# Kernel optimization log

Hardware: AMD Instinct MI355X
Metric: run time of the kernel (lower is better)

## Reference

```python
import jax, jax.numpy as jnp
import numpy as np

NUM_HEADS = 16
GROUP_SIZE = 4
RMS_EPS = 1e-6


def _rope_cos_sin(S, head_dim):
    # matches compute_freqs_cis: freqs = 1/10000**(arange(0,hd,2)/hd), angles = outer(t, freqs)
    inv_freq = 1.0 / (10000.0 ** (jnp.arange(0, head_dim, 2, dtype=jnp.float32) / head_dim))
    t = jnp.arange(S, dtype=jnp.float32)
    angles = t[:, None] * inv_freq[None, :]          # [S, hd/2]
    return jnp.cos(angles), jnp.sin(angles)


def _apply_rope(x, cos, sin):
    # x: [B, S, h, hd]; complex multiply on (even, odd) pairs
    B, S, h, hd = x.shape
    xr = x.reshape(B, S, h, hd // 2, 2)
    x0, x1 = xr[..., 0], xr[..., 1]
    c = cos[None, :, None, :]
    s = sin[None, :, None, :]
    o0 = x0 * c - x1 * s
    o1 = x0 * s + x1 * c
    return jnp.stack([o0, o1], axis=-1).reshape(B, S, h, hd)


def setup_inputs() -> dict:
    key = jax.random.key(0)
    k1, k2, k3 = jax.random.split(key, 3)
    B, S, H = 4, 2048, 2048
    g = GROUP_SIZE
    x = jax.random.normal(k1, (B, S, H), dtype=jnp.float32)
    w_attn = jax.random.normal(k2, (H, H + 2 * H // g), dtype=jnp.float32) * 0.02
    w_proj = jax.random.normal(k3, (H, H), dtype=jnp.float32) * 0.02
    norm_w = jnp.ones((H,), dtype=jnp.float32)
    return {"x": x, "w_attn": w_attn, "w_proj": w_proj, "norm_w": norm_w}


def reference(x, w_attn, w_proj, norm_w):
    B, S, H = x.shape
    nh = NUM_HEADS
    g = GROUP_SIZE
    nkv = nh // g
    hd = H // nh
    ghd = H // g

    qkv = jnp.einsum('bsh,hf->bsf', x, w_attn)
    q = qkv[..., :H].reshape(B, S, nh, hd)
    k = qkv[..., H:H + ghd].reshape(B, S, nkv, hd)
    v = qkv[..., H + ghd:].reshape(B, S, nkv, hd)

    cos, sin = _rope_cos_sin(S, hd)
    q = _apply_rope(q, cos, sin)
    k = _apply_rope(k, cos, sin)

    q = q.transpose(0, 2, 1, 3)                      # [B, nh, S, hd]
    k = jnp.repeat(k.transpose(0, 2, 1, 3), g, axis=1)   # [B, nh, S, hd]
    v = jnp.repeat(v.transpose(0, 2, 1, 3), g, axis=1)

    scale = 1.0 / jnp.sqrt(jnp.float32(hd))
    scores = jnp.einsum('bhqd,bhkd->bhqk', q, k) * scale
    causal = jnp.tril(jnp.ones((S, S), dtype=bool))
    scores = jnp.where(causal[None, None], scores, jnp.finfo(scores.dtype).min)
    attn = jax.nn.softmax(scores, axis=-1)
    y = jnp.einsum('bhqk,bhkd->bhqd', attn, v)       # [B, nh, S, hd]
    y = y.transpose(0, 2, 1, 3).reshape(B, S, H)

    y = jnp.einsum('bsh,ho->bso', y, w_proj)
    # RMSNorm
    rms = jnp.sqrt(jnp.mean(jnp.square(y), axis=-1, keepdims=True) + RMS_EPS)
    return (y / rms) * norm_w
```

## Files before the change

kernel.cpp:

```cpp
#include <hip/hip_runtime.h>

#define DEVI __device__ __forceinline__

using u16 = unsigned short;
using u32 = unsigned int;

typedef __attribute__((ext_vector_type(8))) short short8v;
typedef __attribute__((ext_vector_type(4))) float f32x4;
typedef __attribute__((ext_vector_type(2))) u32 u32x2;

DEVI u16 f2b(float f) {
  u32 u = __builtin_bit_cast(u32, f);
  u += 0x7fffu + ((u >> 16) & 1u);
  return (u16)(u >> 16);
}
DEVI float b2f(u16 b) { return __builtin_bit_cast(float, (u32)b << 16); }

DEVI void gload16(const void* g, void* l) {
  __builtin_amdgcn_global_load_lds(
      (const __attribute__((address_space(1))) void*)g,
      (__attribute__((address_space(3))) void*)l, 16, 0, 0);
}

__global__ __launch_bounds__(256) void cvt_x_k(const float* __restrict__ in,
                                               u16* __restrict__ out) {
  size_t i = ((size_t)blockIdx.x * 256 + threadIdx.x) * 8;
  f32x4 a = *(const f32x4*)(in + i);
  f32x4 c = *(const f32x4*)(in + i + 4);
  short8v o;
  o[0] = (short)f2b(a[0]); o[1] = (short)f2b(a[1]);
  o[2] = (short)f2b(a[2]); o[3] = (short)f2b(a[3]);
  o[4] = (short)f2b(c[0]); o[5] = (short)f2b(c[1]);
  o[6] = (short)f2b(c[2]); o[7] = (short)f2b(c[3]);
  *(short8v*)(out + i) = o;
}

__global__ __launch_bounds__(256) void transpose_cvt_k(
    const float* __restrict__ in, u16* __restrict__ out, int R, int Ccols) {
  __shared__ u16 tile[64][65];
  const int r0 = blockIdx.y * 64, c0 = blockIdx.x * 64;
  const int tx = threadIdx.x & 63, ty = threadIdx.x >> 6;
#pragma unroll
  for (int jj = 0; jj < 16; ++jj) {
    int r = ty + jj * 4;
    tile[r][tx] = f2b(in[(size_t)(r0 + r) * Ccols + c0 + tx]);
  }
  __syncthreads();
#pragma unroll
  for (int jj = 0; jj < 16; ++jj) {
    int c = ty + jj * 4;
    out[(size_t)(c0 + c) * R + r0 + tx] = tile[tx][c];
  }
}

__global__ __launch_bounds__(256) void rope_table_k(float* __restrict__ cosT,
                                                    float* __restrict__ sinT) {
  int idx = blockIdx.x * 256 + threadIdx.x;
  int s = idx >> 6, i = idx & 63;
  float inv_freq = expf(-(float)i * (1.0f / 64.0f) * 9.210340371976184f);
  float ang = (float)s * inv_freq;
  cosT[idx] = cosf(ang);
  sinT[idx] = sinf(ang);
}

__global__ __launch_bounds__(256) void rope_scatter_k(
    const u16* __restrict__ qkv, const float* __restrict__ cosT,
    const float* __restrict__ sinT, u16* __restrict__ q_r,
    u16* __restrict__ k_r) {
  const float QS = 0.08838834764831845f * 1.4426950408889634f;
  const int row = blockIdx.x;
  const int b = row >> 11, s = row & 2047;
  const u16* in = qkv + (size_t)row * 3072;
  const float* cp = cosT + s * 64;
  const float* sp = sinT + s * 64;
  for (int p = threadIdx.x; p < 1280; p += 256) {
    int f0 = p * 2;
    u32 pair = *(const u32*)(in + f0);
    float x0 = b2f((u16)(pair & 0xffffu));
    float x1 = b2f((u16)(pair >> 16));
    int d, head;
    u16* dst;
    bool isq = (f0 < 2048);
    if (isq) {
      head = f0 >> 7; d = f0 & 127;
      dst = q_r + (((size_t)(b * 16 + head)) * 2048 + s) * 128 + d;
    } else {
      int idx = f0 - 2048;
      head = idx >> 7; d = idx & 127;
      dst = k_r + (((size_t)(b * 4 + head)) * 2048 + s) * 128 + d;
    }
    int i = d >> 1;
    float c = cp[i], sn = sp[i];
    float o0 = x0 * c - x1 * sn;
    float o1 = x0 * sn + x1 * c;
    if (isq) { o0 *= QS; o1 *= QS; }
    *(u32*)dst = (u32)f2b(o0) | ((u32)f2b(o1) << 16);
  }
}

__global__ __launch_bounds__(256) void v_trans_k(const u16* __restrict__ qkv,
                                                 u16* __restrict__ vT) {
  __shared__ u16 tile[64][65];
  const int s0 = blockIdx.x * 64, d0 = blockIdx.y * 64;
  const int bk = blockIdx.z;
  const int b = bk >> 2, kh = bk & 3;
  const int tx = threadIdx.x & 63, ty = threadIdx.x >> 6;
  const u16* src = qkv + ((size_t)b * 2048) * 3072 + 2560 + kh * 128;
#pragma unroll
  for (int jj = 0; jj < 16; ++jj) {
    int s = ty + jj * 4;
    tile[s][tx] = src[(size_t)(s0 + s) * 3072 + d0 + tx];
  }
  __syncthreads();
  u16* dst = vT + (((size_t)bk * 128 + d0) * 2048) + s0;
#pragma unroll
  for (int jj = 0; jj < 16; ++jj) {
    int dd = ty + jj * 4;
    dst[(size_t)dd * 2048 + tx] = tile[tx][dd];
  }
}

__global__ __launch_bounds__(256) void gemm_bt_k(const u16* __restrict__ A,
                                                 const u16* __restrict__ BT,
                                                 u16* __restrict__ C, int M,
                                                 int N, int Kd) {
  __shared__ __align__(16) u16 lA[128 * 32];
  __shared__ __align__(16) u16 lB[128 * 32];
  const int t = threadIdx.x;
  const int lane = t & 63, lo = lane & 15, hi = lane >> 4;
  const int w = t >> 6, wm = w >> 1, wn = w & 1;

  const int ntx = gridDim.x;
  const int nwg = ntx * gridDim.y;
  const int orig = blockIdx.y * ntx + blockIdx.x;
  const int cpx = nwg >> 3;
  const int swz = (orig & 7) * cpx + (orig >> 3);
  const int m0 = (swz / ntx) * 128, n0 = (swz % ntx) * 128;

  const int srow = t >> 2, sslot = t & 3;

  f32x4 acc[4][4];
#pragma unroll
  for (int a = 0; a < 4; ++a)
#pragma unroll
    for (int c = 0; c < 4; ++c) acc[a][c] = (f32x4){0.f, 0.f, 0.f, 0.f};

  const int nk = Kd >> 5;
  for (int kt = 0; kt < nk; ++kt) {
    const int k0 = kt << 5;
    __syncthreads();
#pragma unroll
    for (int i = 0; i < 2; ++i) {
      int r = i * 64 + srow;
      int gs = sslot ^ (r & 3);
      gload16((const char*)A + ((size_t)(m0 + r) * Kd + k0 + gs * 8) * 2,
              (char*)lA + i * 4096 + w * 1024);
    }
#pragma unroll
    for (int i = 0; i < 2; ++i) {
      int r = i * 64 + srow;
      int gs = sslot ^ (r & 3);
      gload16((const char*)BT + ((size_t)(n0 + r) * Kd + k0 + gs * 8) * 2,
              (char*)lB + i * 4096 + w * 1024);
    }
    __syncthreads();

    short8v af[4], bfv[4];
#pragma unroll
    for (int mt = 0; mt < 4; ++mt) {
      int r = wm * 64 + mt * 16 + lo;
      af[mt] = *(const short8v*)((const char*)lA + r * 64 + ((hi ^ (r & 3)) << 4));
    }
#pragma unroll
    for (int nt = 0; nt < 4; ++nt) {
      int r = wn * 64 + nt * 16 + lo;
      bfv[nt] = *(const short8v*)((const char*)lB + r * 64 + ((hi ^ (r & 3)) << 4));
    }
    __builtin_amdgcn_s_setprio(1);
#pragma unroll
    for (int mt = 0; mt < 4; ++mt)
#pragma unroll
      for (int nt = 0; nt < 4; ++nt)
        acc[mt][nt] = __builtin_amdgcn_mfma_f32_16x16x32_bf16(
            af[mt], bfv[nt], acc[mt][nt], 0, 0, 0);
    __builtin_amdgcn_s_setprio(0);
  }

#pragma unroll
  for (int mt = 0; mt < 4; ++mt)
#pragma unroll
    for (int nt = 0; nt < 4; ++nt)
#pragma unroll
      for (int r = 0; r < 4; ++r) {
        int row = m0 + wm * 64 + mt * 16 + hi * 4 + r;
        int col = n0 + wn * 64 + nt * 16 + lo;
        C[(size_t)row * N + col] = f2b(acc[mt][nt][r]);
      }
}

__global__ __launch_bounds__(256, 2) void attn_k(const u16* __restrict__ Q,
                                                 const u16* __restrict__ K,
                                                 const u16* __restrict__ VT,
                                                 u16* __restrict__ Y) {
  __shared__ __align__(16) u16 lK[2][64 * 128];
  __shared__ __align__(16) u16 lV[2][128 * 64];
  __shared__ __align__(16) u16 lP[4][32 * 64];

  const int t = threadIdx.x;
  const int lane = t & 63, lo = lane & 15, hi = lane >> 4;
  const int w = t >> 6;
  const int L = lo & 7;

  const int id = blockIdx.x;
  const int xcd = id & 7, pos = id >> 3;
  const int bh = xcd + ((pos >> 4) << 3);
  const int qt = 15 - (pos & 15);
  const int b = bh >> 4, h = bh & 15, kh = h >> 2;

  const size_t qbase = (size_t)(b * 16 + h) * 2048 * 128;
  const size_t kbase = (size_t)(b * 4 + kh) * 2048 * 128;
  const size_t vbase = (size_t)(b * 4 + kh) * 128 * 2048;

  const int q0 = qt * 128;
  const int wq0 = q0 + w * 32;

  short8v qf[2][4];
#pragma unroll
  for (int j2 = 0; j2 < 2; ++j2)
#pragma unroll
    for (int ks = 0; ks < 4; ++ks)
      qf[j2][ks] = *(const short8v*)(Q + qbase +
                                     (size_t)(wq0 + j2 * 16 + lo) * 128 +
                                     ks * 32 + hi * 8);

  float m_run[2], l_run[2];
  m_run[0] = -3.0e38f; m_run[1] = -3.0e38f;
  l_run[0] = 0.f; l_run[1] = 0.f;
  f32x4 oacc[2][8];
#pragma unroll
  for (int j2 = 0; j2 < 2; ++j2)
#pragma unroll
    for (int ot = 0; ot < 8; ++ot) oacc[j2][ot] = (f32x4){0.f, 0.f, 0.f, 0.f};

  const int ntile = 2 * qt + 2;

  auto stage = [&](int buf, int j) {
    const int kv0 = j * 64;
#pragma unroll
    for (int i = 0; i < 4; ++i) {
      int off = i * 4096 + t * 16;
      int r = off >> 8;
      int sl = (off >> 4) & 15;
      int gs = sl ^ (r & 7);
      gload16((const char*)K + (kbase + (size_t)(kv0 + r) * 128 + gs * 8) * 2,
              (char*)lK[buf] + i * 4096 + w * 1024);
    }
#pragma unroll
    for (int i = 0; i < 4; ++i) {
      int off = i * 4096 + t * 16;
      int r = off >> 7;
      int sl = (off >> 4) & 7;
      int gs = sl ^ (r & 7);
      gload16((const char*)VT + (vbase + (size_t)r * 2048 + kv0 + gs * 8) * 2,
              (char*)lV[buf] + i * 4096 + w * 1024);
    }
  };

  stage(0, 0);
  __syncthreads();

  u16* pw = lP[w];

  for (int jj = 0; jj < ntile; ++jj) {
    const int cur = jj & 1;
    if (jj + 1 < ntile) stage(cur ^ 1, jj + 1);

    const u16* lKc = lK[cur];
    const u16* lVc = lV[cur];
    const int kv0 = jj * 64;

    f32x4 sacc[2][4];
#pragma unroll
    for (int j2 = 0; j2 < 2; ++j2)
#pragma unroll
      for (int kt = 0; kt < 4; ++kt) sacc[j2][kt] = (f32x4){0.f, 0.f, 0.f, 0.f};
    __builtin_amdgcn_s_setprio(1);
#pragma unroll
    for (int ks = 0; ks < 4; ++ks) {
#pragma unroll
      for (int kt = 0; kt < 4; ++kt) {
        int kr = kt * 16 + lo;
        int sl = (ks * 4 + hi) ^ (kr & 7);
        short8v kf = *(const short8v*)((const char*)lKc + kr * 256 + (sl << 4));
        sacc[0][kt] = __builtin_amdgcn_mfma_f32_16x16x32_bf16(kf, qf[0][ks],
                                                              sacc[0][kt], 0, 0, 0);
        sacc[1][kt] = __builtin_amdgcn_mfma_f32_16x16x32_bf16(kf, qf[1][ks],
                                                              sacc[1][kt], 0, 0, 0);
      }
    }
    __builtin_amdgcn_s_setprio(0);

    if (jj >= ntile - 2) {
      const int kb = kv0 + hi * 4 - wq0 - lo;
#pragma unroll
      for (int j2 = 0; j2 < 2; ++j2)
#pragma unroll
        for (int kt = 0; kt < 4; ++kt)
#pragma unroll
          for (int r = 0; r < 4; ++r)
            if (kb + kt * 16 + r - j2 * 16 > 0) sacc[j2][kt][r] = -1.0e38f;
    }

    float pmax[2];
#pragma unroll
    for (int j2 = 0; j2 < 2; ++j2) {
      f32x4 m4;
#pragma unroll
      for (int r = 0; r < 4; ++r)
        m4[r] = fmaxf(fmaxf(sacc[j2][0][r], sacc[j2][1][r]),
                      fmaxf(sacc[j2][2][r], sacc[j2][3][r]));
      float m = fmaxf(fmaxf(m4[0], m4[1]), fmaxf(m4[2], m4[3]));
      m = fmaxf(m, __shfl_xor(m, 16, 64));
      m = fmaxf(m, __shfl_xor(m, 32, 64));
      pmax[j2] = m;
    }

    bool need = (pmax[0] > m_run[0] + 8.f) || (pmax[1] > m_run[1] + 8.f);
    if (__any(need)) {
      float corr[2];
#pragma unroll
      for (int j2 = 0; j2 < 2; ++j2) {
        float mn = fmaxf(m_run[j2], pmax[j2]);
        corr[j2] = exp2f(m_run[j2] - mn);
        m_run[j2] = mn;
        l_run[j2] *= corr[j2];
      }
#pragma unroll
      for (int j2 = 0; j2 < 2; ++j2) {
        float c0 = __shfl(corr[j2], hi * 4 + 0, 64);
        float c1 = __shfl(corr[j2], hi * 4 + 1, 64);
        float c2 = __shfl(corr[j2], hi * 4 + 2, 64);
        float c3 = __shfl(corr[j2], hi * 4 + 3, 64);
#pragma unroll
        for (int ot = 0; ot < 8; ++ot) {
          oacc[j2][ot][0] *= c0;
          oacc[j2][ot][1] *= c1;
          oacc[j2][ot][2] *= c2;
          oacc[j2][ot][3] *= c3;
        }
      }
    }

#pragma unroll
    for (int j2 = 0; j2 < 2; ++j2) {
      const float rowm = m_run[j2];
      float s0 = 0.f, s1 = 0.f, s2 = 0.f, s3 = 0.f;
#pragma unroll
      for (int kt = 0; kt < 4; ++kt) {
        float p0 = exp2f(sacc[j2][kt][0] - rowm);
        float p1 = exp2f(sacc[j2][kt][1] - rowm);
        float p2 = exp2f(sacc[j2][kt][2] - rowm);
        float p3 = exp2f(sacc[j2][kt][3] - rowm);
        s0 += p0; s1 += p1; s2 += p2; s3 += p3;
        u32 w0, w1;
        asm("v_cvt_pk_bf16_f32 %0, %1, %2" : "=v"(w0) : "v"(p0), "v"(p1));
        asm("v_cvt_pk_bf16_f32 %0, %1, %2" : "=v"(w1) : "v"(p2), "v"(p3));
        int idx = (j2 * 16 + lo) * 64 + ((kt * 16 + hi * 4) ^ (L << 3));
        *(u32x2*)(pw + idx) = (u32x2){w0, w1};
      }
      float sm = (s0 + s1) + (s2 + s3);
      sm += __shfl_xor(sm, 16, 64);
      sm += __shfl_xor(sm, 32, 64);
      l_run[j2] += sm;
    }

    __builtin_amdgcn_s_setprio(1);
#pragma unroll
    for (int ks = 0; ks < 2; ++ks) {
      short8v pa0 = *(const short8v*)((const char*)pw + (0 * 16 + lo) * 128 +
                                      ((ks * 64 + hi * 16) ^ (L << 4)));
      short8v pa1 = *(const short8v*)((const char*)pw + (16 + lo) * 128 +
                                      ((ks * 64 + hi * 16) ^ (L << 4)));
#pragma unroll
      for (int ot = 0; ot < 8; ++ot) {
        int vr = ot * 16 + lo;
        int sl = (ks * 4 + hi) ^ (vr & 7);
        short8v vf = *(const short8v*)((const char*)lVc + vr * 128 + (sl << 4));
        oacc[0][ot] =
            __builtin_amdgcn_mfma_f32_16x16x32_bf16(pa0, vf, oacc[0][ot], 0, 0, 0);
        oacc[1][ot] =
            __builtin_amdgcn_mfma_f32_16x16x32_bf16(pa1, vf, oacc[1][ot], 0, 0, 0);
      }
    }
    __builtin_amdgcn_s_setprio(0);

    __syncthreads();
  }

  float inv[2][4];
#pragma unroll
  for (int j2 = 0; j2 < 2; ++j2)
#pragma unroll
    for (int r = 0; r < 4; ++r) {
      float lv = __shfl(l_run[j2], hi * 4 + r, 64);
      inv[j2][r] = 1.0f / lv;
    }
#pragma unroll
  for (int j2 = 0; j2 < 2; ++j2)
#pragma unroll
    for (int ot = 0; ot < 8; ++ot)
#pragma unroll
      for (int r = 0; r < 4; ++r) {
        int qrow = wq0 + j2 * 16 + hi * 4 + r;
        Y[((size_t)b * 2048 + qrow) * 2048 + h * 128 + ot * 16 + lo] =
            f2b(oacc[j2][ot][r] * inv[j2][r]);
      }
}

__global__ __launch_bounds__(256) void rmsnorm_k(const u16* __restrict__ Yb,
                                                 const float* __restrict__ nw,
                                                 float* __restrict__ out) {
  const int row = blockIdx.x;
  const int t = threadIdx.x;
  const u16* yr = Yb + (size_t)row * 2048 + t * 8;
  short8v v = *(const short8v*)yr;
  float x[8];
  float ss = 0.f;
#pragma unroll
  for (int j = 0; j < 8; ++j) {
    x[j] = b2f((u16)v[j]);
    ss += x[j] * x[j];
  }
#pragma unroll
  for (int dm = 1; dm < 64; dm <<= 1) ss += __shfl_xor(ss, dm, 64);
  __shared__ float red[4];
  if ((t & 63) == 0) red[t >> 6] = ss;
  __syncthreads();
  float tot = red[0] + red[1] + red[2] + red[3];
  float inv = rsqrtf(tot * (1.0f / 2048.0f) + 1e-6f);
  float* op = out + (size_t)row * 2048 + t * 8;
  const float* wp = nw + t * 8;
  f32x4 o0, o1;
#pragma unroll
  for (int j = 0; j < 4; ++j) o0[j] = x[j] * inv * wp[j];
#pragma unroll
  for (int j = 0; j < 4; ++j) o1[j] = x[4 + j] * inv * wp[4 + j];
  *(f32x4*)op = o0;
  *(f32x4*)(op + 4) = o1;
}

extern "C" void kernel_launch(void* const* d_in, const int* in_sizes, int n_in,
                              void* d_out, int out_size, void* d_ws,
                              size_t ws_size, hipStream_t stream) {
  (void)in_sizes; (void)n_in; (void)out_size; (void)ws_size;
  const float* x = (const float*)d_in[0];
  const float* w_attn = (const float*)d_in[1];
  const float* w_proj = (const float*)d_in[2];
  const float* norm_w = (const float*)d_in[3];
  float* out = (float*)d_out;
  char* ws = (char*)d_ws;

  size_t off = 0;
  auto alloc = [&](size_t n) {
    size_t r = off;
    off += (n + 255) & ~(size_t)255;
    return r;
  };
  u16* xb = (u16*)(ws + alloc(33554432));
  u16* wabT = (u16*)(ws + alloc(12582912));
  u16* qkv = (u16*)(ws + alloc(50331648));
  u16* q_r = (u16*)(ws + alloc(33554432));
  u16* vT = (u16*)(ws + alloc(8388608));
  u16* wpT = (u16*)(ws + alloc(8388608));
  float* cosT = (float*)(ws + alloc(524288));
  float* sinT = (float*)(ws + alloc(524288));
  u16* k_r = wabT;
  u16* y = xb;
  u16* y2 = qkv;

  cvt_x_k<<<8192, 256, 0, stream>>>(x, xb);
  transpose_cvt_k<<<dim3(48, 32), 256, 0, stream>>>(w_attn, wabT, 2048, 3072);
  transpose_cvt_k<<<dim3(32, 32), 256, 0, stream>>>(w_proj, wpT, 2048, 2048);
  rope_table_k<<<512, 256, 0, stream>>>(cosT, sinT);
  gemm_bt_k<<<dim3(24, 64), 256, 0, stream>>>(xb, wabT, qkv, 8192, 3072, 2048);
  rope_scatter_k<<<8192, 256, 0, stream>>>(qkv, cosT, sinT, q_r, k_r);
  v_trans_k<<<dim3(32, 2, 16), 256, 0, stream>>>(qkv, vT);
  attn_k<<<dim3(1024), 256, 0, stream>>>(q_r, k_r, vT, y);
  gemm_bt_k<<<dim3(16, 64), 256, 0, stream>>>(y, wpT, y2, 8192, 2048, 2048);
  rmsnorm_k<<<8192, 256, 0, stream>>>(y2, norm_w, out);
}
```

Baseline: 449.3 us.

## Replace GEMM with 256x256 multi-stage pipelined kernel and shrink attention KV tile

Both projection GEMMs move to a new 512-thread kernel with 256x256 output tiles, 128KB of LDS, and a four-slot global-to-LDS prefetch pipeline. Explicit vmcnt waits and barriers interleave the loads with MFMA phases. The aim is more operand reuse per tile and hidden memory latency, where the old kernel used single-buffered 128x128 tiles. Separately, attention drops the KV tile from 64 to 32 rows and raises the occupancy hint to 3 blocks per CU, trading more loop iterations and barriers for higher occupancy.

```diff
diff --git a/kernel.cpp b/kernel.cpp
--- a/kernel.cpp
+++ b/kernel.cpp
@@ -120,96 +120,131 @@
   }
 }
 
-__global__ __launch_bounds__(256) void gemm_bt_k(const u16* __restrict__ A,
-                                                 const u16* __restrict__ BT,
-                                                 u16* __restrict__ C, int M,
-                                                 int N, int Kd) {
-  __shared__ __align__(16) u16 lA[128 * 32];
-  __shared__ __align__(16) u16 lB[128 * 32];
+DEVI short8v ldf(const char* half, int r, int slot) {
+  return *(const short8v*)(half + r * 64 + (((slot) ^ (r & 3)) << 4));
+}
+
+DEVI void stg(const u16* __restrict__ G, int row0, int Kd, int T, int kh,
+              char* dst, int t, int w) {
+#pragma unroll
+  for (int i = 0; i < 2; ++i) {
+    int off = i * 8192 + t * 16;
+    int r = off >> 6;
+    int gs = ((off >> 4) & 3) ^ (r & 3);
+    gload16((const char*)G +
+                (((size_t)(row0 + r) * Kd) + T * 64 + kh * 32 + gs * 8) * 2,
+            dst + i * 8192 + w * 1024);
+  }
+}
+
+#define VM4 asm volatile("s_waitcnt vmcnt(4)" ::: "memory")
+#define PH(P2, KS, CH, STAGE_STMT, TAILWAIT)                                   \
+  {                                                                            \
+    if ((CH) == 0) {                                                           \
+      _Pragma("unroll") for (int mt = 0; mt < 8; ++mt) af[mt] =                \
+          ldf(Ab + (P2) * 32768 + (KS) * 16384, wm * 128 + mt * 16 + lo, hi);  \
+    }                                                                          \
+    bf0 = ldf(Bb + (P2) * 32768 + (KS) * 16384, wn * 64 + (CH) * 32 + lo, hi);\
+    bf1 = ldf(Bb + (P2) * 32768 + (KS) * 16384,                                \
+              wn * 64 + (CH) * 32 + 16 + lo, hi);                              \
+    STAGE_STMT;                                                                \
+    __builtin_amdgcn_sched_barrier(0);                                         \
+    __builtin_amdgcn_s_barrier();                                              \
+    asm volatile("s_waitcnt lgkmcnt(0)" ::: "memory");                         \
+    __builtin_amdgcn_sched_barrier(0);                                         \
+    __builtin_amdgcn_s_setprio(1);                                             \
+    _Pragma("unroll") for (int mt = 0; mt < 8; ++mt) {                         \
+      acc[mt][(CH) * 2] = __builtin_amdgcn_mfma_f32_16x16x32_bf16(             \
+          af[mt], bf0, acc[mt][(CH) * 2], 0, 0, 0);                            \
+      acc[mt][(CH) * 2 + 1] = __builtin_amdgcn_mfma_f32_16x16x32_bf16(         \
+          af[mt], bf1, acc[mt][(CH) * 2 + 1], 0, 0, 0);                        \
+    }                                                                          \
+    __builtin_amdgcn_s_setprio(0);                                             \
+    TAILWAIT;                                                                  \
+    __builtin_amdgcn_sched_barrier(0);                                         \
+    __builtin_amdgcn_s_barrier();                                              \
+    __builtin_amdgcn_sched_barrier(0);                                         \
+  }
+
+__global__ __launch_bounds__(512, 2) void gemm256_k(const u16* __restrict__ A,
+                                                    const u16* __restrict__ BT,
+                                                    u16* __restrict__ C, int N,
+                                                    int Kd) {
+  __shared__ __align__(16) char lds[131072];
+  char* Ab = lds;
+  char* Bb = lds + 65536;
+
   const int t = threadIdx.x;
   const int lane = t & 63, lo = lane & 15, hi = lane >> 4;
-  const int w = t >> 6, wm = w >> 1, wn = w & 1;
+  const int w = t >> 6, wm = w >> 2, wn = w & 3;
 
   const int ntx = gridDim.x;
   const int nwg = ntx * gridDim.y;
   const int orig = blockIdx.y * ntx + blockIdx.x;
   const int cpx = nwg >> 3;
   const int swz = (orig & 7) * cpx + (orig >> 3);
-  const int m0 = (swz / ntx) * 128, n0 = (swz % ntx) * 128;
-
-  const int srow = t >> 2, sslot = t & 3;
-
-  f32x4 acc[4][4];
-#pragma unroll
-  for (int a = 0; a < 4; ++a)
+  const int m0 = (swz / ntx) * 256, n0 = (swz % ntx) * 256;
+
+  f32x4 acc[8][4];
+#pragma unroll
+  for (int a = 0; a < 8; ++a)
 #pragma unroll
     for (int c = 0; c < 4; ++c) acc[a][c] = (f32x4){0.f, 0.f, 0.f, 0.f};
 
-  const int nk = Kd >> 5;
-  for (int kt = 0; kt < nk; ++kt) {
-    const int k0 = kt << 5;
-    __syncthreads();
-#pragma unroll
-    for (int i = 0; i < 2; ++i) {
-      int r = i * 64 + srow;
-      int gs = sslot ^ (r & 3);
-      gload16((const char*)A + ((size_t)(m0 + r) * Kd + k0 + gs * 8) * 2,
-              (char*)lA + i * 4096 + w * 1024);
-    }
-#pragma unroll
-    for (int i = 0; i < 2; ++i) {
-      int r = i * 64 + srow;
-      int gs = sslot ^ (r & 3);
-      gload16((const char*)BT + ((size_t)(n0 + r) * Kd + k0 + gs * 8) * 2,
-              (char*)lB + i * 4096 + w * 1024);
-    }
-    __syncthreads();
-
-    short8v af[4], bfv[4];
-#pragma unroll
-    for (int mt = 0; mt < 4; ++mt) {
-      int r = wm * 64 + mt * 16 + lo;
-      af[mt] = *(const short8v*)((const char*)lA + r * 64 + ((hi ^ (r & 3)) << 4));
-    }
-#pragma unroll
-    for (int nt = 0; nt < 4; ++nt) {
-      int r = wn * 64 + nt * 16 + lo;
-      bfv[nt] = *(const short8v*)((const char*)lB + r * 64 + ((hi ^ (r & 3)) << 4));
-    }
-    __builtin_amdgcn_s_setprio(1);
-#pragma unroll
-    for (int mt = 0; mt < 4; ++mt)
-#pragma unroll
-      for (int nt = 0; nt < 4; ++nt)
-        acc[mt][nt] = __builtin_amdgcn_mfma_f32_16x16x32_bf16(
-            af[mt], bfv[nt], acc[mt][nt], 0, 0, 0);
-    __builtin_amdgcn_s_setprio(0);
-  }
-
-#pragma unroll
-  for (int mt = 0; mt < 4; ++mt)
+  short8v af[8], bf0, bf1;
+
+  const int NK = Kd >> 6;
+  const int NK2 = NK >> 1;
+
+  stg(A, m0, Kd, 0, 0, Ab + 0, t, w);
+  stg(BT, n0, Kd, 0, 0, Bb + 0, t, w);
+  stg(A, m0, Kd, 0, 1, Ab + 16384, t, w);
+  stg(BT, n0, Kd, 0, 1, Bb + 16384, t, w);
+  stg(A, m0, Kd, 1, 0, Ab + 32768, t, w);
+  stg(BT, n0, Kd, 1, 0, Bb + 32768, t, w);
+  VM4;
+  __builtin_amdgcn_sched_barrier(0);
+  __builtin_amdgcn_s_barrier();
+  __builtin_amdgcn_sched_barrier(0);
+
+  for (int kt2 = 0; kt2 < NK2; ++kt2) {
+    int T1v = 2 * kt2 + 1;
+    int T2v = 2 * kt2 + 2; if (T2v > NK - 1) T2v = NK - 1;
+    int T3v = 2 * kt2 + 3; if (T3v > NK - 1) T3v = NK - 1;
+    PH(0, 0, 0, stg(A, m0, Kd, T1v, 1, Ab + 49152, t, w), (void)0);
+    PH(0, 0, 1, stg(BT, n0, Kd, T1v, 1, Bb + 49152, t, w), (void)0);
+    PH(0, 1, 0, stg(A, m0, Kd, T2v, 0, Ab + 0, t, w), (void)0);
+    PH(0, 1, 1, stg(BT, n0, Kd, T2v, 0, Bb + 0, t, w), VM4);
+    PH(1, 0, 0, stg(A, m0, Kd, T2v, 1, Ab + 16384, t, w), (void)0);
+    PH(1, 0, 1, stg(BT, n0, Kd, T2v, 1, Bb + 16384, t, w), (void)0);
+    PH(1, 1, 0, stg(A, m0, Kd, T3v, 0, Ab + 32768, t, w), (void)0);
+    PH(1, 1, 1, stg(BT, n0, Kd, T3v, 0, Bb + 32768, t, w), VM4);
+  }
+  asm volatile("s_waitcnt vmcnt(0)" ::: "memory");
+
+#pragma unroll
+  for (int mt = 0; mt < 8; ++mt)
 #pragma unroll
     for (int nt = 0; nt < 4; ++nt)
 #pragma unroll
       for (int r = 0; r < 4; ++r) {
-        int row = m0 + wm * 64 + mt * 16 + hi * 4 + r;
+        int row = m0 + wm * 128 + mt * 16 + hi * 4 + r;
         int col = n0 + wn * 64 + nt * 16 + lo;
         C[(size_t)row * N + col] = f2b(acc[mt][nt][r]);
       }
 }
 
-__global__ __launch_bounds__(256, 2) void attn_k(const u16* __restrict__ Q,
+__global__ __launch_bounds__(256, 3) void attn_k(const u16* __restrict__ Q,
                                                  const u16* __restrict__ K,
                                                  const u16* __restrict__ VT,
                                                  u16* __restrict__ Y) {
-  __shared__ __align__(16) u16 lK[2][64 * 128];
-  __shared__ __align__(16) u16 lV[2][128 * 64];
-  __shared__ __align__(16) u16 lP[4][32 * 64];
+  __shared__ __align__(16) u16 lK[2][32 * 128];
+  __shared__ __align__(16) u16 lV[2][128 * 32];
+  __shared__ __align__(16) u16 lP[4][32 * 32];
 
   const int t = threadIdx.x;
   const int lane = t & 63, lo = lane & 15, hi = lane >> 4;
   const int w = t >> 6;
-  const int L = lo & 7;
 
   const int id = blockIdx.x;
   const int xcd = id & 7, pos = id >> 3;
@@ -242,12 +277,12 @@
 #pragma unroll
     for (int ot = 0; ot < 8; ++ot) oacc[j2][ot] = (f32x4){0.f, 0.f, 0.f, 0.f};
 
-  const int ntile = 2 * qt + 2;
+  const int ntile = 4 * qt + 4;
 
   auto stage = [&](int buf, int j) {
-    const int kv0 = j * 64;
-#pragma unroll
-    for (int i = 0; i < 4; ++i) {
+    const int kv0 = j * 32;
+#pragma unroll
+    for (int i = 0; i < 2; ++i) {
       int off = i * 4096 + t * 16;
       int r = off >> 8;
       int sl = (off >> 4) & 15;
@@ -256,11 +291,11 @@
               (char*)lK[buf] + i * 4096 + w * 1024);
     }
 #pragma unroll
-    for (int i = 0; i < 4; ++i) {
+    for (int i = 0; i < 2; ++i) {
       int off = i * 4096 + t * 16;
-      int r = off >> 7;
-      int sl = (off >> 4) & 7;
-      int gs = sl ^ (r & 7);
+      int r = off >> 6;
+      int sl = (off >> 4) & 3;
+      int gs = sl ^ (r & 3);
       gload16((const char*)VT + (vbase + (size_t)r * 2048 + kv0 + gs * 8) * 2,
               (char*)lV[buf] + i * 4096 + w * 1024);
     }
@@ -277,18 +312,18 @@
 
     const u16* lKc = lK[cur];
     const u16* lVc = lV[cur];
-    const int kv0 = jj * 64;
-
-    f32x4 sacc[2][4];
+    const int kv0 = jj * 32;
+
+    f32x4 sacc[2][2];
 #pragma unroll
     for (int j2 = 0; j2 < 2; ++j2)
 #pragma unroll
-      for (int kt = 0; kt < 4; ++kt) sacc[j2][kt] = (f32x4){0.f, 0.f, 0.f, 0.f};
+      for (int kt = 0; kt < 2; ++kt) sacc[j2][kt] = (f32x4){0.f, 0.f, 0.f, 0.f};
     __builtin_amdgcn_s_setprio(1);
 #pragma unroll
     for (int ks = 0; ks < 4; ++ks) {
 #pragma unroll
-      for (int kt = 0; kt < 4; ++kt) {
+      for (int kt = 0; kt < 2; ++kt) {
         int kr = kt * 16 + lo;
         int sl = (ks * 4 + hi) ^ (kr & 7);
         short8v kf = *(const short8v*)((const char*)lKc + kr * 256 + (sl << 4));
@@ -300,12 +335,12 @@
     }
     __builtin_amdgcn_s_setprio(0);
 
-    if (jj >= ntile - 2) {
+    if (jj >= ntile - 4) {
       const int kb = kv0 + hi * 4 - wq0 - lo;
 #pragma unroll
       for (int j2 = 0; j2 < 2; ++j2)
 #pragma unroll
-        for (int kt = 0; kt < 4; ++kt)
+        for (int kt = 0; kt < 2; ++kt)
 #pragma unroll
           for (int r = 0; r < 4; ++r)
             if (kb + kt * 16 + r - j2 * 16 > 0) sacc[j2][kt][r] = -1.0e38f;
@@ -316,9 +351,7 @@
     for (int j2 = 0; j2 < 2; ++j2) {
       f32x4 m4;
 #pragma unroll
-      for (int r = 0; r < 4; ++r)
-        m4[r] = fmaxf(fmaxf(sacc[j2][0][r], sacc[j2][1][r]),
-                      fmaxf(sacc[j2][2][r], sacc[j2][3][r]));
+      for (int r = 0; r < 4; ++r) m4[r] = fmaxf(sacc[j2][0][r], sacc[j2][1][r]);
       float m = fmaxf(fmaxf(m4[0], m4[1]), fmaxf(m4[2], m4[3]));
       m = fmaxf(m, __shfl_xor(m, 16, 64));
       m = fmaxf(m, __shfl_xor(m, 32, 64));
@@ -356,7 +389,7 @@
       const float rowm = m_run[j2];
       float s0 = 0.f, s1 = 0.f, s2 = 0.f, s3 = 0.f;
 #pragma unroll
-      for (int kt = 0; kt < 4; ++kt) {
+      for (int kt = 0; kt < 2; ++kt) {
         float p0 = exp2f(sacc[j2][kt][0] - rowm);
         float p1 = exp2f(sacc[j2][kt][1] - rowm);
         float p2 = exp2f(sacc[j2][kt][2] - rowm);
@@ -365,8 +398,8 @@
         u32 w0, w1;
         asm("v_cvt_pk_bf16_f32 %0, %1, %2" : "=v"(w0) : "v"(p0), "v"(p1));
         asm("v_cvt_pk_bf16_f32 %0, %1, %2" : "=v"(w1) : "v"(p2), "v"(p3));
-        int idx = (j2 * 16 + lo) * 64 + ((kt * 16 + hi * 4) ^ (L << 3));
-        *(u32x2*)(pw + idx) = (u32x2){w0, w1};
+        int byte = ((((kt * 2 + (hi >> 1)) ^ (lo & 3)) << 4) | ((hi & 1) << 3));
+        *(u32x2*)((char*)pw + (j2 * 16 + lo) * 64 + byte) = (u32x2){w0, w1};
       }
       float sm = (s0 + s1) + (s2 + s3);
       sm += __shfl_xor(sm, 16, 64);
@@ -375,17 +408,16 @@
     }
 
     __builtin_amdgcn_s_setprio(1);
-#pragma unroll
-    for (int ks = 0; ks < 2; ++ks) {
-      short8v pa0 = *(const short8v*)((const char*)pw + (0 * 16 + lo) * 128 +
-                                      ((ks * 64 + hi * 16) ^ (L << 4)));
-      short8v pa1 = *(const short8v*)((const char*)pw + (16 + lo) * 128 +
-                                      ((ks * 64 + hi * 16) ^ (L << 4)));
+    {
+      short8v pa0 = *(const short8v*)((const char*)pw + lo * 64 +
+                                      ((hi ^ (lo & 3)) << 4));
+      short8v pa1 = *(const short8v*)((const char*)pw + (16 + lo) * 64 +
+                                      ((hi ^ (lo & 3)) << 4));
 #pragma unroll
       for (int ot = 0; ot < 8; ++ot) {
         int vr = ot * 16 + lo;
-        int sl = (ks * 4 + hi) ^ (vr & 7);
-        short8v vf = *(const short8v*)((const char*)lVc + vr * 128 + (sl << 4));
+        int sl = hi ^ (vr & 3);
+        short8v vf = *(const short8v*)((const char*)lVc + vr * 64 + (sl << 4));
         oacc[0][ot] =
             __builtin_amdgcn_mfma_f32_16x16x32_bf16(pa0, vf, oacc[0][ot], 0, 0, 0);
         oacc[1][ot] =
@@ -482,10 +514,10 @@
   transpose_cvt_k<<<dim3(48, 32), 256, 0, stream>>>(w_attn, wabT, 2048, 3072);
   transpose_cvt_k<<<dim3(32, 32), 256, 0, stream>>>(w_proj, wpT, 2048, 2048);
   rope_table_k<<<512, 256, 0, stream>>>(cosT, sinT);
-  gemm_bt_k<<<dim3(24, 64), 256, 0, stream>>>(xb, wabT, qkv, 8192, 3072, 2048);
+  gemm256_k<<<dim3(12, 32), 512, 0, stream>>>(xb, wabT, qkv, 3072, 2048);
   rope_scatter_k<<<8192, 256, 0, stream>>>(qkv, cosT, sinT, q_r, k_r);
   v_trans_k<<<dim3(32, 2, 16), 256, 0, stream>>>(qkv, vT);
   attn_k<<<dim3(1024), 256, 0, stream>>>(q_r, k_r, vT, y);
-  gemm_bt_k<<<dim3(16, 64), 256, 0, stream>>>(y, wpT, y2, 8192, 2048, 2048);
+  gemm256_k<<<dim3(8, 32), 512, 0, stream>>>(y, wpT, y2, 2048, 2048);
   rmsnorm_k<<<8192, 256, 0, stream>>>(y2, norm_w, out);
 }
```

New measurement: 428.1 us. 1.05x faster.
